# Kernel tuning notes

Hardware: AMD Instinct MI355X
Metric: run time of the kernel (lower is better)

The kernel has to match this reference:

```python
import jax, jax.numpy as jnp
import numpy as np

N = 50000   # num_entities
E = 600000  # num_edges
D = 128     # dim
R = 200     # num_relations
T = 1000    # num_timestamps
L = 2       # num_layers


def setup_inputs() -> dict:
    key = jax.random.key(0)
    ks = jax.random.split(key, 16)
    edge_index = jax.random.randint(ks[0], (2, E), 0, N)
    edge_type = jax.random.randint(ks[1], (E,), 0, R)
    edge_time = jax.random.randint(ks[2], (E,), 0, T)
    edge_weight = jax.random.uniform(ks[3], (E,), dtype=jnp.float32)
    perm = jax.random.permutation(ks[4], N)
    entity_emb = jax.random.normal(ks[5], (N, D), dtype=jnp.float32)
    rel_emb = jax.random.normal(ks[6], (R, D), dtype=jnp.float32)
    time_emb = jax.random.normal(ks[7], (T, D), dtype=jnp.float32)
    s = 1.0 / np.sqrt(D)
    in_proj_w = jax.random.uniform(ks[8], (L, D, 2 * D), minval=-s, maxval=s)
    in_proj_b = jax.random.uniform(ks[9], (L, 2 * D), minval=-s, maxval=s)
    out_proj_w = jax.random.uniform(ks[10], (L, D, D), minval=-s, maxval=s)
    out_proj_b = jax.random.uniform(ks[11], (L, D), minval=-s, maxval=s)
    A = jax.random.normal(ks[12], (L, D)) * 0.1
    B = jax.random.normal(ks[13], (L, D)) * 0.1
    ln_g = jnp.ones((L, D), dtype=jnp.float32)
    ln_b = jnp.zeros((L, D), dtype=jnp.float32)
    return dict(edge_index=edge_index, edge_type=edge_type, edge_time=edge_time,
                edge_weight=edge_weight, perm=perm, entity_emb=entity_emb,
                rel_emb=rel_emb, time_emb=time_emb, in_proj_w=in_proj_w,
                in_proj_b=in_proj_b, out_proj_w=out_proj_w, out_proj_b=out_proj_b,
                A=A, B=B, ln_g=ln_g, ln_b=ln_b)


def _mamba_layer(x, Wi, bi, Wo, bo, A, B, g_ln, b_ln):
    # x: [N, D]
    zg = x @ Wi + bi                      # [N, 2D]
    z, g = jnp.split(zg, 2, axis=-1)
    g = jax.nn.sigmoid(g)

    def step(prev, zg_i):
        z_i, g_i = zg_i
        curr = g_i * (A * prev) + B * z_i
        return curr, curr

    _, h = jax.lax.scan(step, jnp.zeros((D,), x.dtype), (z, g))  # [N, D]
    y = x + h @ Wo + bo
    mu = jnp.mean(y, axis=-1, keepdims=True)
    var = jnp.mean((y - mu) ** 2, axis=-1, keepdims=True)
    return (y - mu) / jnp.sqrt(var + 1e-5) * g_ln + b_ln


def reference(edge_index, edge_type, edge_time, edge_weight, perm, entity_emb,
              rel_emb, time_emb, in_proj_w, in_proj_b, out_proj_w, out_proj_b,
              A, B, ln_g, ln_b):
    src, dst = edge_index[0], edge_index[1]
    msgs = entity_emb[src] + rel_emb[edge_type] + time_emb[edge_time]  # [E, D]
    sums = jax.ops.segment_sum(msgs * edge_weight[:, None], dst, num_segments=N)
    cnt = jax.ops.segment_sum(edge_weight, dst, num_segments=N)
    x = sums / jnp.maximum(cnt, 1.0)[:, None]          # scatter_mean
    x = x / jnp.maximum(jnp.linalg.norm(x, axis=1, keepdims=True), 1e-12)
    x = x[perm]
    for l in range(L):
        x = _mamba_layer(x, in_proj_w[l], in_proj_b[l], out_proj_w[l],
                         out_proj_b[l], A[l], B[l], ln_g[l], ln_b[l])
    return x
```

## Files before the change

### kernel.cpp

```cpp
#include <hip/hip_runtime.h>
#include <hip/hip_bf16.h>

typedef unsigned short ushort_t;
typedef unsigned int   uint_t;
typedef __attribute__((ext_vector_type(8))) short bf8;
typedef __attribute__((ext_vector_type(4))) float f32x4;

constexpr int N = 50000;
constexpr int E = 600000;
constexpr int D = 128;
constexpr int L = 2;
constexpr int NB = (N + 255) / 256;

constexpr int TR   = 48;
constexpr int LOOK = 16;
constexpr int NBLK = (N + TR - 1) / TR;
constexpr int HSTR = 136;

__device__ __forceinline__ float us2f(ushort_t u) {
    union { uint_t i; float f; } c; c.i = (uint_t)u << 16; return c.f;
}
__device__ __forceinline__ ushort_t f2us(float f) {
    __hip_bfloat16 b = __float2bfloat16(f);
    return *(ushort_t*)&b;
}

__global__ __launch_bounds__(256) void k_hist(
    const int* __restrict__ dstp, int* __restrict__ hist)
{
    int e = blockIdx.x * 256 + threadIdx.x;
    if (e < E) atomicAdd(&hist[dstp[e]], 1);
}

__global__ __launch_bounds__(256) void k_scan1(
    const int* __restrict__ hist, int* __restrict__ part, int* __restrict__ bsum)
{
    int i = blockIdx.x * 256 + threadIdx.x;
    int v = (i < N) ? hist[i] : 0;
    int lane = threadIdx.x & 63, wv = threadIdx.x >> 6;
    int s = v;
    #pragma unroll
    for (int m = 1; m < 64; m <<= 1) {
        int t = __shfl_up(s, m, 64);
        if (lane >= m) s += t;
    }
    __shared__ int wsum[4];
    if (lane == 63) wsum[wv] = s;
    __syncthreads();
    int off = 0;
    for (int w = 0; w < wv; w++) off += wsum[w];
    if (i < N) part[i] = s - v + off;
    if (threadIdx.x == 255)
        bsum[blockIdx.x] = wsum[0] + wsum[1] + wsum[2] + wsum[3];
}

__global__ __launch_bounds__(256) void k_scan2(int* __restrict__ bsum)
{
    int i = threadIdx.x;
    int v = (i < NB) ? bsum[i] : 0;
    int lane = i & 63, wv = i >> 6;
    int s = v;
    #pragma unroll
    for (int m = 1; m < 64; m <<= 1) {
        int t = __shfl_up(s, m, 64);
        if (lane >= m) s += t;
    }
    __shared__ int wsum[4];
    if (lane == 63) wsum[wv] = s;
    __syncthreads();
    int off = 0;
    for (int w = 0; w < wv; w++) off += wsum[w];
    if (i < NB) bsum[i] = s - v + off;
}

__global__ __launch_bounds__(256) void k_finalize(
    const int* __restrict__ part, const int* __restrict__ bsum,
    int* __restrict__ cursor, int* __restrict__ rowst,
    const int* __restrict__ perm, int* __restrict__ invp)
{
    int i = blockIdx.x * 256 + threadIdx.x;
    if (i < N) {
        int b = part[i] + bsum[i >> 8];
        cursor[i] = b;
        rowst[i] = b;
        invp[perm[i]] = i;
    }
}

__global__ __launch_bounds__(256) void k_scatter(
    const int* __restrict__ eidx, const int* __restrict__ etype,
    const int* __restrict__ etime, const float* __restrict__ ew,
    int* __restrict__ cursor, int2* __restrict__ esort)
{
    int e = blockIdx.x * 256 + threadIdx.x;
    if (e >= E) return;
    int dst = eidx[E + e];
    int slot = atomicAdd(&cursor[dst], 1);
    int2 p;
    p.x = (eidx[e] & 0xffff) | (etype[e] << 16);
    p.y = (etime[e] & 0xffff) | ((int)f2us(ew[e]) << 16);
    esort[slot] = p;
}

__global__ __launch_bounds__(256) void k_cast(
    const float* __restrict__ ent, const float* __restrict__ rel,
    const float* __restrict__ tim, const float* __restrict__ Wi,
    const float* __restrict__ Wo, ushort_t* __restrict__ entb,
    ushort_t* __restrict__ relb, ushort_t* __restrict__ timb,
    ushort_t* __restrict__ WiT, ushort_t* __restrict__ WoT)
{
    size_t t = (size_t)blockIdx.x * 256 + threadIdx.x;
    if (t < 3276800) {
        const float2* s; uint_t* d; size_t off;
        if (t < 3200000)      { s = (const float2*)ent; d = (uint_t*)entb; off = t; }
        else if (t < 3212800) { s = (const float2*)rel; d = (uint_t*)relb; off = t - 3200000; }
        else                  { s = (const float2*)tim; d = (uint_t*)timb; off = t - 3212800; }
        float2 v = s[off];
        d[off] = (uint_t)f2us(v.x) | ((uint_t)f2us(v.y) << 16);
    } else {
        size_t u = t - 3276800;
        if (u < (size_t)L * 256 * 128) {
            int l = u / (256 * 128), r = u % (256 * 128);
            int n = r / 128, k = r % 128;
            WiT[u] = f2us(Wi[(size_t)l * 128 * 256 + k * 256 + n]);
        } else if (u < (size_t)L * 256 * 128 + L * 128 * 128) {
            size_t v = u - (size_t)L * 256 * 128;
            int l = v / (128 * 128), r = v % (128 * 128);
            int n = r / 128, k = r % 128;
            WoT[v] = f2us(Wo[(size_t)l * 128 * 128 + k * 128 + n]);
        }
    }
}

__global__ __launch_bounds__(256) void k_agg(
    const int2* __restrict__ esort, const int* __restrict__ rowst,
    const int* __restrict__ hist, const int* __restrict__ invp,
    const ushort_t* __restrict__ entb, const ushort_t* __restrict__ relb,
    const ushort_t* __restrict__ timb, ushort_t* __restrict__ xbf)
{
    int wv = threadIdx.x >> 6, lane = threadIdx.x & 63;
    int d = blockIdx.x * 4 + wv;
    if (d >= N) return;
    int beg = rowst[d];
    int n = hist[d];

    float s0[4] = {0.f, 0.f, 0.f, 0.f};
    float s1[4] = {0.f, 0.f, 0.f, 0.f};
    float sw[4] = {0.f, 0.f, 0.f, 0.f};

    int j = 0;
    for (; j + 3 < n; j += 4) {
        int2 rec[4];
        #pragma unroll
        for (int u = 0; u < 4; u++) rec[u] = esort[beg + j + u];
        #pragma unroll
        for (int u = 0; u < 4; u++) {
            int  sA = rec[u].x & 0xffff, tA = ((uint_t)rec[u].x) >> 16;
            int  mA = rec[u].y & 0xffff;
            float w = us2f((ushort_t)(((uint_t)rec[u].y) >> 16));
            uint_t va = *(const uint_t*)(entb + (size_t)sA * D + 2 * lane);
            uint_t vb = *(const uint_t*)(relb + (size_t)tA * D + 2 * lane);
            uint_t vc = *(const uint_t*)(timb + (size_t)mA * D + 2 * lane);
            s0[u] += (us2f(va & 0xffff) + us2f(vb & 0xffff) + us2f(vc & 0xffff)) * w;
            s1[u] += (us2f(va >> 16)    + us2f(vb >> 16)    + us2f(vc >> 16))    * w;
            sw[u] += w;
        }
    }
    for (; j < n; j++) {
        int2 p = esort[beg + j];
        int  sA = p.x & 0xffff, tA = ((uint_t)p.x) >> 16;
        int  mA = p.y & 0xffff;
        float w = us2f((ushort_t)(((uint_t)p.y) >> 16));
        uint_t va = *(const uint_t*)(entb + (size_t)sA * D + 2 * lane);
        uint_t vb = *(const uint_t*)(relb + (size_t)tA * D + 2 * lane);
        uint_t vc = *(const uint_t*)(timb + (size_t)mA * D + 2 * lane);
        s0[0] += (us2f(va & 0xffff) + us2f(vb & 0xffff) + us2f(vc & 0xffff)) * w;
        s1[0] += (us2f(va >> 16)    + us2f(vb >> 16)    + us2f(vc >> 16))    * w;
        sw[0] += w;
    }
    float a0 = (s0[0] + s0[1]) + (s0[2] + s0[3]);
    float a1 = (s1[0] + s1[1]) + (s1[2] + s1[3]);
    float wsum = (sw[0] + sw[1]) + (sw[2] + sw[3]);

    float inv = 1.0f / fmaxf(wsum, 1.0f);
    a0 *= inv; a1 *= inv;

    float ss = a0 * a0 + a1 * a1;
    #pragma unroll
    for (int m = 32; m >= 1; m >>= 1) ss += __shfl_xor(ss, m, 64);
    float sc = 1.0f / fmaxf(sqrtf(ss), 1e-12f);

    int orow = invp[d];
    uint_t out = (uint_t)f2us(a0 * sc) | ((uint_t)f2us(a1 * sc) << 16);
    *(uint_t*)(xbf + (size_t)orow * D + 2 * lane) = out;
}

template <bool FINAL>
__global__ __launch_bounds__(256, 4) void k_layer(
    const ushort_t* __restrict__ xin, const ushort_t* __restrict__ WiT,
    const float* __restrict__ bi, const ushort_t* __restrict__ WoT,
    const float* __restrict__ bo, const float* __restrict__ Aw,
    const float* __restrict__ Bw, const float* __restrict__ lg,
    const float* __restrict__ lb, ushort_t* __restrict__ xoutb,
    float* __restrict__ outf)
{
    __shared__ ushort_t hs[TR * HSTR];
    __shared__ float redS[TR * 4], redQ[TR * 4], muA[TR], rsA[TR];

    int tid = threadIdx.x;
    int w = tid >> 6, lane = tid & 63;
    int quad = lane >> 4, m = lane & 15;
    int r0 = blockIdx.x * TR;
    int base = r0 - LOOK;

    const bf8 zero8 = {0, 0, 0, 0, 0, 0, 0, 0};
    const f32x4 zero4 = {0.f, 0.f, 0.f, 0.f};

    int cz0 = w * 32 + m;
    int cz1 = cz0 + 16;

    float Ad0 = Aw[cz0], Bd0 = Bw[cz0];
    float Ad1 = Aw[cz1], Bd1 = Bw[cz1];
    float bz0 = bi[cz0], bz1 = bi[cz1];
    float bg0 = bi[cz0 + 128], bg1 = bi[cz1 + 128];

    bf8 Bz0[4], Bz1[4], Bg0[4], Bg1[4];
    {
        int colz0 = w * 32 + m, colz1 = colz0 + 16;
        #pragma unroll
        for (int kb = 0; kb < 4; kb++) {
            int ko = kb * 32 + quad * 8;
            Bz0[kb] = *(const bf8*)(WiT + (size_t)colz0 * 128 + ko);
            Bz1[kb] = *(const bf8*)(WiT + (size_t)colz1 * 128 + ko);
            Bg0[kb] = *(const bf8*)(WiT + (size_t)(colz0 + 128) * 128 + ko);
            Bg1[kb] = *(const bf8*)(WiT + (size_t)(colz1 + 128) * 128 + ko);
        }
    }

    float carry0 = 0.f, carry1 = 0.f;
    for (int rt = 0; rt < 4; rt++) {
        int gr = base + rt * 16 + m;
        bf8 a[4];
        if (gr >= 0 && gr < N) {
            #pragma unroll
            for (int kb = 0; kb < 4; kb++)
                a[kb] = *(const bf8*)(xin + (size_t)gr * 128 + kb * 32 + quad * 8);
        } else {
            #pragma unroll
            for (int kb = 0; kb < 4; kb++) a[kb] = zero8;
        }
        f32x4 az0 = zero4, az1 = zero4, ag0 = zero4, ag1 = zero4;
        #pragma unroll
        for (int kb = 0; kb < 4; kb++) {
            az0 = __builtin_amdgcn_mfma_f32_16x16x32_bf16(a[kb], Bz0[kb], az0, 0, 0, 0);
            az1 = __builtin_amdgcn_mfma_f32_16x16x32_bf16(a[kb], Bz1[kb], az1, 0, 0, 0);
            ag0 = __builtin_amdgcn_mfma_f32_16x16x32_bf16(a[kb], Bg0[kb], ag0, 0, 0, 0);
            ag1 = __builtin_amdgcn_mfma_f32_16x16x32_bf16(a[kb], Bg1[kb], ag1, 0, 0, 0);
        }
        float P0 = 1.f, Q0 = 0.f, P1 = 1.f, Q1 = 0.f;
        #pragma unroll
        for (int reg = 0; reg < 4; reg++) {
            int grr = base + rt * 16 + quad * 4 + reg;
            bool ok = (grr >= 0) && (grr < N);
            float z0 = az0[reg] + bz0, z1 = az1[reg] + bz1;
            float g0 = 1.f / (1.f + __expf(-(ag0[reg] + bg0)));
            float g1 = 1.f / (1.f + __expf(-(ag1[reg] + bg1)));
            float ca0 = ok ? g0 * Ad0 : 0.f, cb0 = ok ? Bd0 * z0 : 0.f;
            float ca1 = ok ? g1 * Ad1 : 0.f, cb1 = ok ? Bd1 * z1 : 0.f;
            az0[reg] = ca0; ag0[reg] = cb0;
            az1[reg] = ca1; ag1[reg] = cb1;
            P0 = ca0 * P0; Q0 = ca0 * Q0 + cb0;
            P1 = ca1 * P1; Q1 = ca1 * Q1 + cb1;
        }
        float Pp, Qp;
        Pp = __shfl_up(P0, 16, 64); Qp = __shfl_up(Q0, 16, 64);
        if (quad >= 1) { Q0 = P0 * Qp + Q0; P0 = P0 * Pp; }
        Pp = __shfl_up(P1, 16, 64); Qp = __shfl_up(Q1, 16, 64);
        if (quad >= 1) { Q1 = P1 * Qp + Q1; P1 = P1 * Pp; }
        Pp = __shfl_up(P0, 32, 64); Qp = __shfl_up(Q0, 32, 64);
        if (quad >= 2) { Q0 = P0 * Qp + Q0; P0 = P0 * Pp; }
        Pp = __shfl_up(P1, 32, 64); Qp = __shfl_up(Q1, 32, 64);
        if (quad >= 2) { Q1 = P1 * Qp + Q1; P1 = P1 * Pp; }
        float Pe0 = __shfl_up(P0, 16, 64), Qe0 = __shfl_up(Q0, 16, 64);
        float Pe1 = __shfl_up(P1, 16, 64), Qe1 = __shfl_up(Q1, 16, 64);
        if (quad == 0) { Pe0 = 1.f; Qe0 = 0.f; Pe1 = 1.f; Qe1 = 0.f; }
        float h0 = Pe0 * carry0 + Qe0;
        float h1 = Pe1 * carry1 + Qe1;
        float Pc0 = __shfl(P0, m + 48, 64), Qc0 = __shfl(Q0, m + 48, 64);
        float Pc1 = __shfl(P1, m + 48, 64), Qc1 = __shfl(Q1, m + 48, 64);
        carry0 = Pc0 * carry0 + Qc0;
        carry1 = Pc1 * carry1 + Qc1;
        #pragma unroll
        for (int reg = 0; reg < 4; reg++) {
            h0 = az0[reg] * h0 + ag0[reg];
            h1 = az1[reg] * h1 + ag1[reg];
            if (rt >= 1) {
                int lrow = (rt - 1) * 16 + quad * 4 + reg;
                hs[lrow * HSTR + cz0] = f2us(h0);
                hs[lrow * HSTR + cz1] = f2us(h1);
            }
        }
    }
    __syncthreads();

    float y[3][2][4];
    {
        int c0 = w * 32 + m, c1 = c0 + 16;
        float bias0 = bo[c0], bias1 = bo[c1];
        bf8 b0[4], b1[4];
        #pragma unroll
        for (int kb = 0; kb < 4; kb++) {
            int ko = kb * 32 + quad * 8;
            b0[kb] = *(const bf8*)(WoT + (size_t)c0 * 128 + ko);
            b1[kb] = *(const bf8*)(WoT + (size_t)c1 * 128 + ko);
        }
        #pragma unroll
        for (int rt = 0; rt < 3; rt++) {
            bf8 a[4];
            #pragma unroll
            for (int kb = 0; kb < 4; kb++)
                a[kb] = *(const bf8*)(hs + (rt * 16 + m) * HSTR + kb * 32 + quad * 8);
            f32x4 acc0 = zero4, acc1 = zero4;
            #pragma unroll
            for (int kb = 0; kb < 4; kb++) {
                acc0 = __builtin_amdgcn_mfma_f32_16x16x32_bf16(a[kb], b0[kb], acc0, 0, 0, 0);
                acc1 = __builtin_amdgcn_mfma_f32_16x16x32_bf16(a[kb], b1[kb], acc1, 0, 0, 0);
            }
            #pragma unroll
            for (int reg = 0; reg < 4; reg++) {
                int gr = r0 + rt * 16 + quad * 4 + reg;
                float r0v = 0.f, r1v = 0.f;
                if (gr < N) {
                    r0v = us2f(xin[(size_t)gr * 128 + c0]);
                    r1v = us2f(xin[(size_t)gr * 128 + c1]);
                }
                y[rt][0][reg] = acc0[reg] + bias0 + r0v;
                y[rt][1][reg] = acc1[reg] + bias1 + r1v;
            }
        }
    }

    {
        #pragma unroll
        for (int rt = 0; rt < 3; rt++)
            #pragma unroll
            for (int reg = 0; reg < 4; reg++) {
                float v0 = y[rt][0][reg], v1 = y[rt][1][reg];
                float s = v0 + v1, q = v0 * v0 + v1 * v1;
                #pragma unroll
                for (int mk = 1; mk <= 8; mk <<= 1) {
                    s += __shfl_xor(s, mk, 64);
                    q += __shfl_xor(q, mk, 64);
                }
                if (m == 0) {
                    int row = rt * 16 + quad * 4 + reg;
                    redS[row * 4 + w] = s;
                    redQ[row * 4 + w] = q;
                }
            }
    }
    __syncthreads();
    if (tid < TR) {
        float s = redS[tid * 4] + redS[tid * 4 + 1] + redS[tid * 4 + 2] + redS[tid * 4 + 3];
        float q = redQ[tid * 4] + redQ[tid * 4 + 1] + redQ[tid * 4 + 2] + redQ[tid * 4 + 3];
        float mu = s * (1.f / 128.f);
        float var = q * (1.f / 128.f) - mu * mu;
        muA[tid] = mu;
        rsA[tid] = rsqrtf(var + 1e-5f);
    }
    __syncthreads();
    {
        int c0 = w * 32 + m, c1 = c0 + 16;
        float gl0 = lg[c0], gl1 = lg[c1], bl0 = lb[c0], bl1 = lb[c1];
        #pragma unroll
        for (int rt = 0; rt < 3; rt++)
            #pragma unroll
            for (int reg = 0; reg < 4; reg++) {
                int rr = rt * 16 + quad * 4 + reg;
                int gr = r0 + rr;
                if (gr < N) {
                    float mu = muA[rr], rs = rsA[rr];
                    float v0 = (y[rt][0][reg] - mu) * rs * gl0 + bl0;
                    float v1 = (y[rt][1][reg] - mu) * rs * gl1 + bl1;
                    if (FINAL) {
                        outf[(size_t)gr * 128 + c0] = v0;
                        outf[(size_t)gr * 128 + c1] = v1;
                    } else {
                        xoutb[(size_t)gr * 128 + c0] = f2us(v0);
                        xoutb[(size_t)gr * 128 + c1] = f2us(v1);
                    }
                }
            }
    }
}

extern "C" void kernel_launch(void* const* d_in, const int* in_sizes, int n_in,
                              void* d_out, int out_size, void* d_ws, size_t ws_size,
                              hipStream_t stream)
{
    const int*   eidx  = (const int*)d_in[0];
    const int*   etype = (const int*)d_in[1];
    const int*   etime = (const int*)d_in[2];
    const float* ew    = (const float*)d_in[3];
    const int*   perm  = (const int*)d_in[4];
    const float* ent   = (const float*)d_in[5];
    const float* rel   = (const float*)d_in[6];
    const float* tim   = (const float*)d_in[7];
    const float* Wi    = (const float*)d_in[8];
    const float* bi    = (const float*)d_in[9];
    const float* Wo    = (const float*)d_in[10];
    const float* bo    = (const float*)d_in[11];
    const float* Aw    = (const float*)d_in[12];
    const float* Bw    = (const float*)d_in[13];
    const float* lg    = (const float*)d_in[14];
    const float* lbp   = (const float*)d_in[15];

    char* base = (char*)d_ws;
    size_t o = 0;
    ushort_t* xbf  = (ushort_t*)(base + o); o += (size_t)N * D * 2;
    ushort_t* xb2  = (ushort_t*)(base + o); o += (size_t)N * D * 2;
    ushort_t* entb = (ushort_t*)(base + o); o += (size_t)N * D * 2;
    ushort_t* relb = (ushort_t*)(base + o); o += (size_t)200 * D * 2;
    ushort_t* timb = (ushort_t*)(base + o); o += (size_t)1000 * D * 2;
    ushort_t* WiT  = (ushort_t*)(base + o); o += (size_t)L * 256 * 128 * 2;
    ushort_t* WoT  = (ushort_t*)(base + o); o += (size_t)L * 128 * 128 * 2;
    int2*     esort  = (int2*)(base + o);   o += (size_t)E * 8;
    int*      hist   = (int*)(base + o);    o += (size_t)N * 4;
    int*      part   = (int*)(base + o);    o += (size_t)N * 4;
    int*      bsum   = (int*)(base + o);    o += 256 * 4;
    int*      cursor = (int*)(base + o);    o += (size_t)N * 4;
    int*      rowst  = (int*)(base + o);    o += (size_t)N * 4;
    int*      invp   = (int*)(base + o);    o += (size_t)N * 4;

    hipMemsetAsync(hist, 0, N * sizeof(int), stream);

    k_cast    <<<13185, 256, 0, stream>>>(ent, rel, tim, Wi, Wo,
                                          entb, relb, timb, WiT, WoT);
    k_hist    <<<(E + 255) / 256, 256, 0, stream>>>(eidx + E, hist);
    k_scan1   <<<NB, 256, 0, stream>>>(hist, part, bsum);
    k_scan2   <<<1, 256, 0, stream>>>(bsum);
    k_finalize<<<NB, 256, 0, stream>>>(part, bsum, cursor, rowst, perm, invp);
    k_scatter <<<(E + 255) / 256, 256, 0, stream>>>(eidx, etype, etime, ew,
                                                    cursor, esort);
    k_agg     <<<(N + 3) / 4, 256, 0, stream>>>(esort, rowst, hist, invp,
                                                entb, relb, timb, xbf);

    k_layer<false><<<NBLK, 256, 0, stream>>>(
        xbf, WiT, bi, WoT, bo, Aw, Bw, lg, lbp, xb2, nullptr);
    k_layer<true><<<NBLK, 256, 0, stream>>>(
        xb2, WiT + (size_t)256 * 128, bi + 256, WoT + (size_t)128 * 128,
        bo + 128, Aw + 128, Bw + 128, lg + 128, lbp + 128,
        nullptr, (float*)d_out);
}
```

Measured before the change: 303.6 us.

## Fuse both Mamba layers into one kernel and use single-pass decoupled-lookback scan

The two per-layer kernels become one fused kernel. It recomputes layer 1 over an extended window with a 32-row lookback, keeps the intermediate x1 in shared memory, then runs layer 2 from shared memory, so the bf16 round trip of x between layers is gone. The three-kernel CSR prefix scan becomes a single decoupled-lookback kernel. The memset is folded into the cast kernel and the invperm build into the histogram kernel. The aggregation loop is unrolled by 8 to keep more gathers in flight. The cost is extra redundant layer-1 rows per tile, more shared memory, and a lookback scan that relies on blocks being scheduled in forward order.

```diff
diff --git a/kernel.cpp b/kernel.cpp
--- a/kernel.cpp
+++ b/kernel.cpp
@@ -3,6 +3,7 @@
 
 typedef unsigned short ushort_t;
 typedef unsigned int   uint_t;
+typedef unsigned long long ull_t;
 typedef __attribute__((ext_vector_type(8))) short bf8;
 typedef __attribute__((ext_vector_type(4))) float f32x4;
 
@@ -13,7 +14,6 @@
 constexpr int NB = (N + 255) / 256;
 
 constexpr int TR   = 48;
-constexpr int LOOK = 16;
 constexpr int NBLK = (N + TR - 1) / TR;
 constexpr int HSTR = 136;
 
@@ -23,83 +23,6 @@
 __device__ __forceinline__ ushort_t f2us(float f) {
     __hip_bfloat16 b = __float2bfloat16(f);
     return *(ushort_t*)&b;
-}
-
-__global__ __launch_bounds__(256) void k_hist(
-    const int* __restrict__ dstp, int* __restrict__ hist)
-{
-    int e = blockIdx.x * 256 + threadIdx.x;
-    if (e < E) atomicAdd(&hist[dstp[e]], 1);
-}
-
-__global__ __launch_bounds__(256) void k_scan1(
-    const int* __restrict__ hist, int* __restrict__ part, int* __restrict__ bsum)
-{
-    int i = blockIdx.x * 256 + threadIdx.x;
-    int v = (i < N) ? hist[i] : 0;
-    int lane = threadIdx.x & 63, wv = threadIdx.x >> 6;
-    int s = v;
-    #pragma unroll
-    for (int m = 1; m < 64; m <<= 1) {
-        int t = __shfl_up(s, m, 64);
-        if (lane >= m) s += t;
-    }
-    __shared__ int wsum[4];
-    if (lane == 63) wsum[wv] = s;
-    __syncthreads();
-    int off = 0;
-    for (int w = 0; w < wv; w++) off += wsum[w];
-    if (i < N) part[i] = s - v + off;
-    if (threadIdx.x == 255)
-        bsum[blockIdx.x] = wsum[0] + wsum[1] + wsum[2] + wsum[3];
-}
-
-__global__ __launch_bounds__(256) void k_scan2(int* __restrict__ bsum)
-{
-    int i = threadIdx.x;
-    int v = (i < NB) ? bsum[i] : 0;
-    int lane = i & 63, wv = i >> 6;
-    int s = v;
-    #pragma unroll
-    for (int m = 1; m < 64; m <<= 1) {
-        int t = __shfl_up(s, m, 64);
-        if (lane >= m) s += t;
-    }
-    __shared__ int wsum[4];
-    if (lane == 63) wsum[wv] = s;
-    __syncthreads();
-    int off = 0;
-    for (int w = 0; w < wv; w++) off += wsum[w];
-    if (i < NB) bsum[i] = s - v + off;
-}
-
-__global__ __launch_bounds__(256) void k_finalize(
-    const int* __restrict__ part, const int* __restrict__ bsum,
-    int* __restrict__ cursor, int* __restrict__ rowst,
-    const int* __restrict__ perm, int* __restrict__ invp)
-{
-    int i = blockIdx.x * 256 + threadIdx.x;
-    if (i < N) {
-        int b = part[i] + bsum[i >> 8];
-        cursor[i] = b;
-        rowst[i] = b;
-        invp[perm[i]] = i;
-    }
-}
-
-__global__ __launch_bounds__(256) void k_scatter(
-    const int* __restrict__ eidx, const int* __restrict__ etype,
-    const int* __restrict__ etime, const float* __restrict__ ew,
-    int* __restrict__ cursor, int2* __restrict__ esort)
-{
-    int e = blockIdx.x * 256 + threadIdx.x;
-    if (e >= E) return;
-    int dst = eidx[E + e];
-    int slot = atomicAdd(&cursor[dst], 1);
-    int2 p;
-    p.x = (eidx[e] & 0xffff) | (etype[e] << 16);
-    p.y = (etime[e] & 0xffff) | ((int)f2us(ew[e]) << 16);
-    esort[slot] = p;
 }
 
 __global__ __launch_bounds__(256) void k_cast(
@@ -107,9 +30,12 @@
     const float* __restrict__ tim, const float* __restrict__ Wi,
     const float* __restrict__ Wo, ushort_t* __restrict__ entb,
     ushort_t* __restrict__ relb, ushort_t* __restrict__ timb,
-    ushort_t* __restrict__ WiT, ushort_t* __restrict__ WoT)
+    ushort_t* __restrict__ WiT, ushort_t* __restrict__ WoT,
+    int* __restrict__ hist, ull_t* __restrict__ state)
 {
     size_t t = (size_t)blockIdx.x * 256 + threadIdx.x;
+    if (t < 12500) ((int4*)hist)[t] = make_int4(0, 0, 0, 0);
+    if (t < (size_t)NB) state[t] = 0ULL;
     if (t < 3276800) {
         const float2* s; uint_t* d; size_t off;
         if (t < 3200000)      { s = (const float2*)ent; d = (uint_t*)entb; off = t; }
@@ -132,6 +58,71 @@
     }
 }
 
+__global__ __launch_bounds__(256) void k_hist(
+    const int* __restrict__ dstp, int* __restrict__ hist,
+    const int* __restrict__ perm, int* __restrict__ invp)
+{
+    int e = blockIdx.x * 256 + threadIdx.x;
+    if (e < E) atomicAdd(&hist[dstp[e]], 1);
+    if (e < N) invp[perm[e]] = e;
+}
+
+__global__ __launch_bounds__(256) void k_scanp(
+    const int* __restrict__ hist, ull_t* __restrict__ state,
+    int* __restrict__ cursor, int* __restrict__ rowst)
+{
+    int b = blockIdx.x;
+    int tid = threadIdx.x;
+    int i = b * 256 + tid;
+    int v = (i < N) ? hist[i] : 0;
+    int lane = tid & 63, wv = tid >> 6;
+    int s = v;
+    #pragma unroll
+    for (int m = 1; m < 64; m <<= 1) {
+        int t = __shfl_up(s, m, 64);
+        if (lane >= m) s += t;
+    }
+    __shared__ int wsum[4];
+    __shared__ int baseSh;
+    if (lane == 63) wsum[wv] = s;
+    __syncthreads();
+    int off = 0;
+    for (int w = 0; w < wv; w++) off += wsum[w];
+    int total = wsum[0] + wsum[1] + wsum[2] + wsum[3];
+
+    if (tid == 0) {
+        atomicExch(&state[b], (1ULL << 62) | (uint_t)total);
+        long long excl = 0;
+        for (int p = b - 1; p >= 0; ) {
+            ull_t st;
+            do { st = atomicAdd(&state[p], 0ULL); } while ((st >> 62) == 0);
+            excl += (uint_t)st;
+            if ((st >> 62) == 2ULL) break;
+            p--;
+        }
+        atomicExch(&state[b], (2ULL << 62) | (uint_t)(excl + total));
+        baseSh = (int)excl;
+    }
+    __syncthreads();
+    int ex = baseSh + off + s - v;
+    if (i < N) { cursor[i] = ex; rowst[i] = ex; }
+}
+
+__global__ __launch_bounds__(256) void k_scatter(
+    const int* __restrict__ eidx, const int* __restrict__ etype,
+    const int* __restrict__ etime, const float* __restrict__ ew,
+    int* __restrict__ cursor, int2* __restrict__ esort)
+{
+    int e = blockIdx.x * 256 + threadIdx.x;
+    if (e >= E) return;
+    int dst = eidx[E + e];
+    int slot = atomicAdd(&cursor[dst], 1);
+    int2 p;
+    p.x = (eidx[e] & 0xffff) | (etype[e] << 16);
+    p.y = (etime[e] & 0xffff) | ((int)f2us(ew[e]) << 16);
+    esort[slot] = p;
+}
+
 __global__ __launch_bounds__(256) void k_agg(
     const int2* __restrict__ esort, const int* __restrict__ rowst,
     const int* __restrict__ hist, const int* __restrict__ invp,
@@ -149,6 +140,24 @@
     float sw[4] = {0.f, 0.f, 0.f, 0.f};
 
     int j = 0;
+    for (; j + 7 < n; j += 8) {
+        int2 rec[8];
+        #pragma unroll
+        for (int u = 0; u < 8; u++) rec[u] = esort[beg + j + u];
+        #pragma unroll
+        for (int u = 0; u < 8; u++) {
+            int  sA = rec[u].x & 0xffff, tA = ((uint_t)rec[u].x) >> 16;
+            int  mA = rec[u].y & 0xffff;
+            float w = us2f((ushort_t)(((uint_t)rec[u].y) >> 16));
+            uint_t va = *(const uint_t*)(entb + (size_t)sA * D + 2 * lane);
+            uint_t vb = *(const uint_t*)(relb + (size_t)tA * D + 2 * lane);
+            uint_t vc = *(const uint_t*)(timb + (size_t)mA * D + 2 * lane);
+            int bk = u & 3;
+            s0[bk] += (us2f(va & 0xffff) + us2f(vb & 0xffff) + us2f(vc & 0xffff)) * w;
+            s1[bk] += (us2f(va >> 16)    + us2f(vb >> 16)    + us2f(vc >> 16))    * w;
+            sw[bk] += w;
+        }
+    }
     for (; j + 3 < n; j += 4) {
         int2 rec[4];
         #pragma unroll
@@ -195,127 +204,137 @@
     *(uint_t*)(xbf + (size_t)orow * D + 2 * lane) = out;
 }
 
-template <bool FINAL>
-__global__ __launch_bounds__(256, 4) void k_layer(
+__device__ __forceinline__ void tile_scan(
+    f32x4& az0, f32x4& az1, f32x4& ag0, f32x4& ag1,
+    float bz0, float bz1, float bg0, float bg1,
+    float Ad0, float Bd0, float Ad1, float Bd1,
+    int rowStart, int quad, int m,
+    float& carry0, float& carry1, float h0o[4], float h1o[4])
+{
+    float P0 = 1.f, Q0 = 0.f, P1 = 1.f, Q1 = 0.f;
+    #pragma unroll
+    for (int reg = 0; reg < 4; reg++) {
+        int grr = rowStart + quad * 4 + reg;
+        bool ok = (grr >= 0) && (grr < N);
+        float z0 = az0[reg] + bz0, z1 = az1[reg] + bz1;
+        float g0 = 1.f / (1.f + __expf(-(ag0[reg] + bg0)));
+        float g1 = 1.f / (1.f + __expf(-(ag1[reg] + bg1)));
+        float ca0 = ok ? g0 * Ad0 : 0.f, cb0 = ok ? Bd0 * z0 : 0.f;
+        float ca1 = ok ? g1 * Ad1 : 0.f, cb1 = ok ? Bd1 * z1 : 0.f;
+        az0[reg] = ca0; ag0[reg] = cb0;
+        az1[reg] = ca1; ag1[reg] = cb1;
+        P0 = ca0 * P0; Q0 = ca0 * Q0 + cb0;
+        P1 = ca1 * P1; Q1 = ca1 * Q1 + cb1;
+    }
+    float Pp, Qp;
+    Pp = __shfl_up(P0, 16, 64); Qp = __shfl_up(Q0, 16, 64);
+    if (quad >= 1) { Q0 = P0 * Qp + Q0; P0 = P0 * Pp; }
+    Pp = __shfl_up(P1, 16, 64); Qp = __shfl_up(Q1, 16, 64);
+    if (quad >= 1) { Q1 = P1 * Qp + Q1; P1 = P1 * Pp; }
+    Pp = __shfl_up(P0, 32, 64); Qp = __shfl_up(Q0, 32, 64);
+    if (quad >= 2) { Q0 = P0 * Qp + Q0; P0 = P0 * Pp; }
+    Pp = __shfl_up(P1, 32, 64); Qp = __shfl_up(Q1, 32, 64);
+    if (quad >= 2) { Q1 = P1 * Qp + Q1; P1 = P1 * Pp; }
+    float Pe0 = __shfl_up(P0, 16, 64), Qe0 = __shfl_up(Q0, 16, 64);
+    float Pe1 = __shfl_up(P1, 16, 64), Qe1 = __shfl_up(Q1, 16, 64);
+    if (quad == 0) { Pe0 = 1.f; Qe0 = 0.f; Pe1 = 1.f; Qe1 = 0.f; }
+    float h0 = Pe0 * carry0 + Qe0;
+    float h1 = Pe1 * carry1 + Qe1;
+    float Pc0 = __shfl(P0, m + 48, 64), Qc0 = __shfl(Q0, m + 48, 64);
+    float Pc1 = __shfl(P1, m + 48, 64), Qc1 = __shfl(Q1, m + 48, 64);
+    carry0 = Pc0 * carry0 + Qc0;
+    carry1 = Pc1 * carry1 + Qc1;
+    #pragma unroll
+    for (int reg = 0; reg < 4; reg++) {
+        h0 = az0[reg] * h0 + ag0[reg];
+        h1 = az1[reg] * h1 + ag1[reg];
+        h0o[reg] = h0; h1o[reg] = h1;
+    }
+}
+
+__global__ __launch_bounds__(256, 4) void k_fused(
     const ushort_t* __restrict__ xin, const ushort_t* __restrict__ WiT,
     const float* __restrict__ bi, const ushort_t* __restrict__ WoT,
     const float* __restrict__ bo, const float* __restrict__ Aw,
     const float* __restrict__ Bw, const float* __restrict__ lg,
-    const float* __restrict__ lb, ushort_t* __restrict__ xoutb,
-    float* __restrict__ outf)
-{
-    __shared__ ushort_t hs[TR * HSTR];
-    __shared__ float redS[TR * 4], redQ[TR * 4], muA[TR], rsA[TR];
+    const float* __restrict__ lb, float* __restrict__ outf)
+{
+    __shared__ ushort_t hs[64 * HSTR];
+    __shared__ ushort_t x1s[64 * HSTR];
+    __shared__ float redS[64 * 4], redQ[64 * 4], muA[64], rsA[64];
 
     int tid = threadIdx.x;
     int w = tid >> 6, lane = tid & 63;
     int quad = lane >> 4, m = lane & 15;
     int r0 = blockIdx.x * TR;
-    int base = r0 - LOOK;
 
     const bf8 zero8 = {0, 0, 0, 0, 0, 0, 0, 0};
     const f32x4 zero4 = {0.f, 0.f, 0.f, 0.f};
 
-    int cz0 = w * 32 + m;
-    int cz1 = cz0 + 16;
-
-    float Ad0 = Aw[cz0], Bd0 = Bw[cz0];
-    float Ad1 = Aw[cz1], Bd1 = Bw[cz1];
-    float bz0 = bi[cz0], bz1 = bi[cz1];
-    float bg0 = bi[cz0 + 128], bg1 = bi[cz1 + 128];
-
-    bf8 Bz0[4], Bz1[4], Bg0[4], Bg1[4];
+    int cz0 = w * 32 + m, cz1 = cz0 + 16;
+
     {
-        int colz0 = w * 32 + m, colz1 = colz0 + 16;
+        int base1 = r0 - 32;
+        float Ad0 = Aw[cz0], Bd0 = Bw[cz0], Ad1 = Aw[cz1], Bd1 = Bw[cz1];
+        float bz0 = bi[cz0], bz1 = bi[cz1];
+        float bg0 = bi[cz0 + 128], bg1 = bi[cz1 + 128];
+        bf8 Bz0[4], Bz1[4], Bg0[4], Bg1[4];
         #pragma unroll
         for (int kb = 0; kb < 4; kb++) {
             int ko = kb * 32 + quad * 8;
-            Bz0[kb] = *(const bf8*)(WiT + (size_t)colz0 * 128 + ko);
-            Bz1[kb] = *(const bf8*)(WiT + (size_t)colz1 * 128 + ko);
-            Bg0[kb] = *(const bf8*)(WiT + (size_t)(colz0 + 128) * 128 + ko);
-            Bg1[kb] = *(const bf8*)(WiT + (size_t)(colz1 + 128) * 128 + ko);
-        }
-    }
-
-    float carry0 = 0.f, carry1 = 0.f;
-    for (int rt = 0; rt < 4; rt++) {
-        int gr = base + rt * 16 + m;
-        bf8 a[4];
-        if (gr >= 0 && gr < N) {
-            #pragma unroll
-            for (int kb = 0; kb < 4; kb++)
-                a[kb] = *(const bf8*)(xin + (size_t)gr * 128 + kb * 32 + quad * 8);
-        } else {
-            #pragma unroll
-            for (int kb = 0; kb < 4; kb++) a[kb] = zero8;
-        }
-        f32x4 az0 = zero4, az1 = zero4, ag0 = zero4, ag1 = zero4;
-        #pragma unroll
-        for (int kb = 0; kb < 4; kb++) {
-            az0 = __builtin_amdgcn_mfma_f32_16x16x32_bf16(a[kb], Bz0[kb], az0, 0, 0, 0);
-            az1 = __builtin_amdgcn_mfma_f32_16x16x32_bf16(a[kb], Bz1[kb], az1, 0, 0, 0);
-            ag0 = __builtin_amdgcn_mfma_f32_16x16x32_bf16(a[kb], Bg0[kb], ag0, 0, 0, 0);
-            ag1 = __builtin_amdgcn_mfma_f32_16x16x32_bf16(a[kb], Bg1[kb], ag1, 0, 0, 0);
-        }
-        float P0 = 1.f, Q0 = 0.f, P1 = 1.f, Q1 = 0.f;
-        #pragma unroll
-        for (int reg = 0; reg < 4; reg++) {
-            int grr = base + rt * 16 + quad * 4 + reg;
-            bool ok = (grr >= 0) && (grr < N);
-            float z0 = az0[reg] + bz0, z1 = az1[reg] + bz1;
-            float g0 = 1.f / (1.f + __expf(-(ag0[reg] + bg0)));
-            float g1 = 1.f / (1.f + __expf(-(ag1[reg] + bg1)));
-            float ca0 = ok ? g0 * Ad0 : 0.f, cb0 = ok ? Bd0 * z0 : 0.f;
-            float ca1 = ok ? g1 * Ad1 : 0.f, cb1 = ok ? Bd1 * z1 : 0.f;
-            az0[reg] = ca0; ag0[reg] = cb0;
-            az1[reg] = ca1; ag1[reg] = cb1;
-            P0 = ca0 * P0; Q0 = ca0 * Q0 + cb0;
-            P1 = ca1 * P1; Q1 = ca1 * Q1 + cb1;
-        }
-        float Pp, Qp;
-        Pp = __shfl_up(P0, 16, 64); Qp = __shfl_up(Q0, 16, 64);
-        if (quad >= 1) { Q0 = P0 * Qp + Q0; P0 = P0 * Pp; }
-        Pp = __shfl_up(P1, 16, 64); Qp = __shfl_up(Q1, 16, 64);
-        if (quad >= 1) { Q1 = P1 * Qp + Q1; P1 = P1 * Pp; }
-        Pp = __shfl_up(P0, 32, 64); Qp = __shfl_up(Q0, 32, 64);
-        if (quad >= 2) { Q0 = P0 * Qp + Q0; P0 = P0 * Pp; }
-        Pp = __shfl_up(P1, 32, 64); Qp = __shfl_up(Q1, 32, 64);
-        if (quad >= 2) { Q1 = P1 * Qp + Q1; P1 = P1 * Pp; }
-        float Pe0 = __shfl_up(P0, 16, 64), Qe0 = __shfl_up(Q0, 16, 64);
-        float Pe1 = __shfl_up(P1, 16, 64), Qe1 = __shfl_up(Q1, 16, 64);
-        if (quad == 0) { Pe0 = 1.f; Qe0 = 0.f; Pe1 = 1.f; Qe1 = 0.f; }
-        float h0 = Pe0 * carry0 + Qe0;
-        float h1 = Pe1 * carry1 + Qe1;
-        float Pc0 = __shfl(P0, m + 48, 64), Qc0 = __shfl(Q0, m + 48, 64);
-        float Pc1 = __shfl(P1, m + 48, 64), Qc1 = __shfl(Q1, m + 48, 64);
-        carry0 = Pc0 * carry0 + Qc0;
-        carry1 = Pc1 * carry1 + Qc1;
-        #pragma unroll
-        for (int reg = 0; reg < 4; reg++) {
-            h0 = az0[reg] * h0 + ag0[reg];
-            h1 = az1[reg] * h1 + ag1[reg];
+            Bz0[kb] = *(const bf8*)(WiT + (size_t)cz0 * 128 + ko);
+            Bz1[kb] = *(const bf8*)(WiT + (size_t)cz1 * 128 + ko);
+            Bg0[kb] = *(const bf8*)(WiT + (size_t)(cz0 + 128) * 128 + ko);
+            Bg1[kb] = *(const bf8*)(WiT + (size_t)(cz1 + 128) * 128 + ko);
+        }
+        float carry0 = 0.f, carry1 = 0.f;
+        for (int rt = 0; rt < 5; rt++) {
+            int gr = base1 + rt * 16 + m;
+            bf8 a[4];
+            if (gr >= 0 && gr < N) {
+                #pragma unroll
+                for (int kb = 0; kb < 4; kb++)
+                    a[kb] = *(const bf8*)(xin + (size_t)gr * 128 + kb * 32 + quad * 8);
+            } else {
+                #pragma unroll
+                for (int kb = 0; kb < 4; kb++) a[kb] = zero8;
+            }
+            f32x4 az0 = zero4, az1 = zero4, ag0 = zero4, ag1 = zero4;
+            #pragma unroll
+            for (int kb = 0; kb < 4; kb++) {
+                az0 = __builtin_amdgcn_mfma_f32_16x16x32_bf16(a[kb], Bz0[kb], az0, 0, 0, 0);
+                az1 = __builtin_amdgcn_mfma_f32_16x16x32_bf16(a[kb], Bz1[kb], az1, 0, 0, 0);
+                ag0 = __builtin_amdgcn_mfma_f32_16x16x32_bf16(a[kb], Bg0[kb], ag0, 0, 0, 0);
+                ag1 = __builtin_amdgcn_mfma_f32_16x16x32_bf16(a[kb], Bg1[kb], ag1, 0, 0, 0);
+            }
+            float h0[4], h1[4];
+            tile_scan(az0, az1, ag0, ag1, bz0, bz1, bg0, bg1,
+                      Ad0, Bd0, Ad1, Bd1, base1 + rt * 16, quad, m,
+                      carry0, carry1, h0, h1);
             if (rt >= 1) {
-                int lrow = (rt - 1) * 16 + quad * 4 + reg;
-                hs[lrow * HSTR + cz0] = f2us(h0);
-                hs[lrow * HSTR + cz1] = f2us(h1);
+                #pragma unroll
+                for (int reg = 0; reg < 4; reg++) {
+                    int lr = (rt - 1) * 16 + quad * 4 + reg;
+                    hs[lr * HSTR + cz0] = f2us(h0[reg]);
+                    hs[lr * HSTR + cz1] = f2us(h1[reg]);
+                }
             }
         }
     }
     __syncthreads();
 
-    float y[3][2][4];
     {
-        int c0 = w * 32 + m, c1 = c0 + 16;
-        float bias0 = bo[c0], bias1 = bo[c1];
+        float bias0 = bo[cz0], bias1 = bo[cz1];
         bf8 b0[4], b1[4];
         #pragma unroll
         for (int kb = 0; kb < 4; kb++) {
             int ko = kb * 32 + quad * 8;
-            b0[kb] = *(const bf8*)(WoT + (size_t)c0 * 128 + ko);
-            b1[kb] = *(const bf8*)(WoT + (size_t)c1 * 128 + ko);
-        }
-        #pragma unroll
-        for (int rt = 0; rt < 3; rt++) {
+            b0[kb] = *(const bf8*)(WoT + (size_t)cz0 * 128 + ko);
+            b1[kb] = *(const bf8*)(WoT + (size_t)cz1 * 128 + ko);
+        }
+        float y1[4][2][4];
+        #pragma unroll
+        for (int rt = 0; rt < 4; rt++) {
             bf8 a[4];
             #pragma unroll
             for (int kb = 0; kb < 4; kb++)
@@ -328,24 +347,21 @@
             }
             #pragma unroll
             for (int reg = 0; reg < 4; reg++) {
-                int gr = r0 + rt * 16 + quad * 4 + reg;
+                int gr = r0 - 16 + rt * 16 + quad * 4 + reg;
                 float r0v = 0.f, r1v = 0.f;
-                if (gr < N) {
-                    r0v = us2f(xin[(size_t)gr * 128 + c0]);
-                    r1v = us2f(xin[(size_t)gr * 128 + c1]);
-                }
-                y[rt][0][reg] = acc0[reg] + bias0 + r0v;
-                y[rt][1][reg] = acc1[reg] + bias1 + r1v;
-            }
-        }
-    }
-
-    {
-        #pragma unroll
-        for (int rt = 0; rt < 3; rt++)
+                if (gr >= 0 && gr < N) {
+                    r0v = us2f(xin[(size_t)gr * 128 + cz0]);
+                    r1v = us2f(xin[(size_t)gr * 128 + cz1]);
+                }
+                y1[rt][0][reg] = acc0[reg] + bias0 + r0v;
+                y1[rt][1][reg] = acc1[reg] + bias1 + r1v;
+            }
+        }
+        #pragma unroll
+        for (int rt = 0; rt < 4; rt++)
             #pragma unroll
             for (int reg = 0; reg < 4; reg++) {
-                float v0 = y[rt][0][reg], v1 = y[rt][1][reg];
+                float v0 = y1[rt][0][reg], v1 = y1[rt][1][reg];
                 float s = v0 + v1, q = v0 * v0 + v1 * v1;
                 #pragma unroll
                 for (int mk = 1; mk <= 8; mk <<= 1) {
@@ -358,20 +374,141 @@
                     redQ[row * 4 + w] = q;
                 }
             }
+        __syncthreads();
+        if (tid < 64) {
+            float s = redS[tid * 4] + redS[tid * 4 + 1] + redS[tid * 4 + 2] + redS[tid * 4 + 3];
+            float q = redQ[tid * 4] + redQ[tid * 4 + 1] + redQ[tid * 4 + 2] + redQ[tid * 4 + 3];
+            float mu = s * (1.f / 128.f);
+            float var = q * (1.f / 128.f) - mu * mu;
+            muA[tid] = mu;
+            rsA[tid] = rsqrtf(var + 1e-5f);
+        }
+        __syncthreads();
+        float gl0 = lg[cz0], gl1 = lg[cz1], bl0 = lb[cz0], bl1 = lb[cz1];
+        #pragma unroll
+        for (int rt = 0; rt < 4; rt++)
+            #pragma unroll
+            for (int reg = 0; reg < 4; reg++) {
+                int row = rt * 16 + quad * 4 + reg;
+                float mu = muA[row], rs = rsA[row];
+                float v0 = (y1[rt][0][reg] - mu) * rs * gl0 + bl0;
+                float v1 = (y1[rt][1][reg] - mu) * rs * gl1 + bl1;
+                x1s[row * HSTR + cz0] = f2us(v0);
+                x1s[row * HSTR + cz1] = f2us(v1);
+            }
     }
     __syncthreads();
-    if (tid < TR) {
-        float s = redS[tid * 4] + redS[tid * 4 + 1] + redS[tid * 4 + 2] + redS[tid * 4 + 3];
-        float q = redQ[tid * 4] + redQ[tid * 4 + 1] + redQ[tid * 4 + 2] + redQ[tid * 4 + 3];
-        float mu = s * (1.f / 128.f);
-        float var = q * (1.f / 128.f) - mu * mu;
-        muA[tid] = mu;
-        rsA[tid] = rsqrtf(var + 1e-5f);
+
+    {
+        const ushort_t* WiT2 = WiT + (size_t)256 * 128;
+        const float* bi2 = bi + 256;
+        float Ad0 = Aw[128 + cz0], Bd0 = Bw[128 + cz0];
+        float Ad1 = Aw[128 + cz1], Bd1 = Bw[128 + cz1];
+        float bz0 = bi2[cz0], bz1 = bi2[cz1];
+        float bg0 = bi2[cz0 + 128], bg1 = bi2[cz1 + 128];
+        bf8 Bz0[4], Bz1[4], Bg0[4], Bg1[4];
+        #pragma unroll
+        for (int kb = 0; kb < 4; kb++) {
+            int ko = kb * 32 + quad * 8;
+            Bz0[kb] = *(const bf8*)(WiT2 + (size_t)cz0 * 128 + ko);
+            Bz1[kb] = *(const bf8*)(WiT2 + (size_t)cz1 * 128 + ko);
+            Bg0[kb] = *(const bf8*)(WiT2 + (size_t)(cz0 + 128) * 128 + ko);
+            Bg1[kb] = *(const bf8*)(WiT2 + (size_t)(cz1 + 128) * 128 + ko);
+        }
+        float carry0 = 0.f, carry1 = 0.f;
+        float h2keep[4][2][4];
+        (void)h2keep;
+        for (int rt = 0; rt < 4; rt++) {
+            bf8 a[4];
+            #pragma unroll
+            for (int kb = 0; kb < 4; kb++)
+                a[kb] = *(const bf8*)(x1s + (rt * 16 + m) * HSTR + kb * 32 + quad * 8);
+            f32x4 az0 = zero4, az1 = zero4, ag0 = zero4, ag1 = zero4;
+            #pragma unroll
+            for (int kb = 0; kb < 4; kb++) {
+                az0 = __builtin_amdgcn_mfma_f32_16x16x32_bf16(a[kb], Bz0[kb], az0, 0, 0, 0);
+                az1 = __builtin_amdgcn_mfma_f32_16x16x32_bf16(a[kb], Bz1[kb], az1, 0, 0, 0);
+                ag0 = __builtin_amdgcn_mfma_f32_16x16x32_bf16(a[kb], Bg0[kb], ag0, 0, 0, 0);
+                ag1 = __builtin_amdgcn_mfma_f32_16x16x32_bf16(a[kb], Bg1[kb], ag1, 0, 0, 0);
+            }
+            float h0[4], h1[4];
+            tile_scan(az0, az1, ag0, ag1, bz0, bz1, bg0, bg1,
+                      Ad0, Bd0, Ad1, Bd1, r0 - 16 + rt * 16, quad, m,
+                      carry0, carry1, h0, h1);
+            if (rt >= 1) {
+                #pragma unroll
+                for (int reg = 0; reg < 4; reg++) {
+                    int lr = (rt - 1) * 16 + quad * 4 + reg;
+                    hs[lr * HSTR + cz0] = f2us(h0[reg]);
+                    hs[lr * HSTR + cz1] = f2us(h1[reg]);
+                }
+            }
+        }
     }
     __syncthreads();
+
     {
-        int c0 = w * 32 + m, c1 = c0 + 16;
-        float gl0 = lg[c0], gl1 = lg[c1], bl0 = lb[c0], bl1 = lb[c1];
+        const ushort_t* WoT2 = WoT + (size_t)128 * 128;
+        const float* bo2 = bo + 128;
+        float bias0 = bo2[cz0], bias1 = bo2[cz1];
+        bf8 b0[4], b1[4];
+        #pragma unroll
+        for (int kb = 0; kb < 4; kb++) {
+            int ko = kb * 32 + quad * 8;
+            b0[kb] = *(const bf8*)(WoT2 + (size_t)cz0 * 128 + ko);
+            b1[kb] = *(const bf8*)(WoT2 + (size_t)cz1 * 128 + ko);
+        }
+        float y2[3][2][4];
+        #pragma unroll
+        for (int rt = 0; rt < 3; rt++) {
+            bf8 a[4];
+            #pragma unroll
+            for (int kb = 0; kb < 4; kb++)
+                a[kb] = *(const bf8*)(hs + (rt * 16 + m) * HSTR + kb * 32 + quad * 8);
+            f32x4 acc0 = zero4, acc1 = zero4;
+            #pragma unroll
+            for (int kb = 0; kb < 4; kb++) {
+                acc0 = __builtin_amdgcn_mfma_f32_16x16x32_bf16(a[kb], b0[kb], acc0, 0, 0, 0);
+                acc1 = __builtin_amdgcn_mfma_f32_16x16x32_bf16(a[kb], b1[kb], acc1, 0, 0, 0);
+            }
+            #pragma unroll
+            for (int reg = 0; reg < 4; reg++) {
+                int lrow = 16 + rt * 16 + quad * 4 + reg;
+                float r0v = us2f(x1s[lrow * HSTR + cz0]);
+                float r1v = us2f(x1s[lrow * HSTR + cz1]);
+                y2[rt][0][reg] = acc0[reg] + bias0 + r0v;
+                y2[rt][1][reg] = acc1[reg] + bias1 + r1v;
+            }
+        }
+        #pragma unroll
+        for (int rt = 0; rt < 3; rt++)
+            #pragma unroll
+            for (int reg = 0; reg < 4; reg++) {
+                float v0 = y2[rt][0][reg], v1 = y2[rt][1][reg];
+                float s = v0 + v1, q = v0 * v0 + v1 * v1;
+                #pragma unroll
+                for (int mk = 1; mk <= 8; mk <<= 1) {
+                    s += __shfl_xor(s, mk, 64);
+                    q += __shfl_xor(q, mk, 64);
+                }
+                if (m == 0) {
+                    int row = rt * 16 + quad * 4 + reg;
+                    redS[row * 4 + w] = s;
+                    redQ[row * 4 + w] = q;
+                }
+            }
+        __syncthreads();
+        if (tid < TR) {
+            float s = redS[tid * 4] + redS[tid * 4 + 1] + redS[tid * 4 + 2] + redS[tid * 4 + 3];
+            float q = redQ[tid * 4] + redQ[tid * 4 + 1] + redQ[tid * 4 + 2] + redQ[tid * 4 + 3];
+            float mu = s * (1.f / 128.f);
+            float var = q * (1.f / 128.f) - mu * mu;
+            muA[tid] = mu;
+            rsA[tid] = rsqrtf(var + 1e-5f);
+        }
+        __syncthreads();
+        float gl0 = lg[128 + cz0], gl1 = lg[128 + cz1];
+        float bl0 = lb[128 + cz0], bl1 = lb[128 + cz1];
         #pragma unroll
         for (int rt = 0; rt < 3; rt++)
             #pragma unroll
@@ -380,15 +517,8 @@
                 int gr = r0 + rr;
                 if (gr < N) {
                     float mu = muA[rr], rs = rsA[rr];
-                    float v0 = (y[rt][0][reg] - mu) * rs * gl0 + bl0;
-                    float v1 = (y[rt][1][reg] - mu) * rs * gl1 + bl1;
-                    if (FINAL) {
-                        outf[(size_t)gr * 128 + c0] = v0;
-                        outf[(size_t)gr * 128 + c1] = v1;
-                    } else {
-                        xoutb[(size_t)gr * 128 + c0] = f2us(v0);
-                        xoutb[(size_t)gr * 128 + c1] = f2us(v1);
-                    }
+                    outf[(size_t)gr * 128 + cz0] = (y2[rt][0][reg] - mu) * rs * gl0 + bl0;
+                    outf[(size_t)gr * 128 + cz1] = (y2[rt][1][reg] - mu) * rs * gl1 + bl1;
                 }
             }
     }
@@ -418,37 +548,26 @@
     char* base = (char*)d_ws;
     size_t o = 0;
     ushort_t* xbf  = (ushort_t*)(base + o); o += (size_t)N * D * 2;
-    ushort_t* xb2  = (ushort_t*)(base + o); o += (size_t)N * D * 2;
     ushort_t* entb = (ushort_t*)(base + o); o += (size_t)N * D * 2;
     ushort_t* relb = (ushort_t*)(base + o); o += (size_t)200 * D * 2;
     ushort_t* timb = (ushort_t*)(base + o); o += (size_t)1000 * D * 2;
     ushort_t* WiT  = (ushort_t*)(base + o); o += (size_t)L * 256 * 128 * 2;
     ushort_t* WoT  = (ushort_t*)(base + o); o += (size_t)L * 128 * 128 * 2;
     int2*     esort  = (int2*)(base + o);   o += (size_t)E * 8;
+    ull_t*    state  = (ull_t*)(base + o);  o += (size_t)NB * 8 + 8;
     int*      hist   = (int*)(base + o);    o += (size_t)N * 4;
-    int*      part   = (int*)(base + o);    o += (size_t)N * 4;
-    int*      bsum   = (int*)(base + o);    o += 256 * 4;
     int*      cursor = (int*)(base + o);    o += (size_t)N * 4;
     int*      rowst  = (int*)(base + o);    o += (size_t)N * 4;
     int*      invp   = (int*)(base + o);    o += (size_t)N * 4;
 
-    hipMemsetAsync(hist, 0, N * sizeof(int), stream);
-
-    k_cast    <<<13185, 256, 0, stream>>>(ent, rel, tim, Wi, Wo,
-                                          entb, relb, timb, WiT, WoT);
-    k_hist    <<<(E + 255) / 256, 256, 0, stream>>>(eidx + E, hist);
-    k_scan1   <<<NB, 256, 0, stream>>>(hist, part, bsum);
-    k_scan2   <<<1, 256, 0, stream>>>(bsum);
-    k_finalize<<<NB, 256, 0, stream>>>(part, bsum, cursor, rowst, perm, invp);
-    k_scatter <<<(E + 255) / 256, 256, 0, stream>>>(eidx, etype, etime, ew,
-                                                    cursor, esort);
-    k_agg     <<<(N + 3) / 4, 256, 0, stream>>>(esort, rowst, hist, invp,
-                                                entb, relb, timb, xbf);
-
-    k_layer<false><<<NBLK, 256, 0, stream>>>(
-        xbf, WiT, bi, WoT, bo, Aw, Bw, lg, lbp, xb2, nullptr);
-    k_layer<true><<<NBLK, 256, 0, stream>>>(
-        xb2, WiT + (size_t)256 * 128, bi + 256, WoT + (size_t)128 * 128,
-        bo + 128, Aw + 128, Bw + 128, lg + 128, lbp + 128,
-        nullptr, (float*)d_out);
-}
+    k_cast   <<<13185, 256, 0, stream>>>(ent, rel, tim, Wi, Wo,
+                                         entb, relb, timb, WiT, WoT, hist, state);
+    k_hist   <<<(E + 255) / 256, 256, 0, stream>>>(eidx + E, hist, perm, invp);
+    k_scanp  <<<NB, 256, 0, stream>>>(hist, state, cursor, rowst);
+    k_scatter<<<(E + 255) / 256, 256, 0, stream>>>(eidx, etype, etime, ew,
+                                                   cursor, esort);
+    k_agg    <<<(N + 3) / 4, 256, 0, stream>>>(esort, rowst, hist, invp,
+                                               entb, relb, timb, xbf);
+    k_fused  <<<NBLK, 256, 0, stream>>>(xbf, WiT, bi, WoT, bo, Aw, Bw,
+                                        lg, lbp, (float*)d_out);
+}
```

After: 306.1 us. No clear change (+0.8%).
